# Optimization experiments

Measured on AMD Instinct MI355X. Metric: run time of the kernel, lower is better.

Reference implementation:

```python
import jax, jax.numpy as jnp
import numpy as np
import math

N_EMBD = 1024
N_HEAD = 16
B, T = 2, 2048


def new_gelu(x):
    # GPT-2 tanh-approx GELU (matches torch module exactly)
    return 0.5 * x * (1.0 + jnp.tanh(jnp.sqrt(2.0 / jnp.pi) * (x + 0.044715 * x ** 3)))


def layer_norm(x, w, b, eps=1e-5):
    mu = jnp.mean(x, axis=-1, keepdims=True)
    var = jnp.var(x, axis=-1, keepdims=True)
    return (x - mu) * jax.lax.rsqrt(var + eps) * w + b


def setup_inputs() -> dict:
    key = jax.random.key(0)
    ks = jax.random.split(key, 8)
    C = N_EMBD
    s = 0.02
    return {
        "x": jax.random.normal(ks[0], (B, T, C), dtype=jnp.float32),
        "ln1_w": jnp.ones((C,), jnp.float32),
        "ln1_b": jnp.zeros((C,), jnp.float32),
        "attn_w": s * jax.random.normal(ks[1], (C, 3 * C), jnp.float32),
        "attn_b": jnp.zeros((3 * C,), jnp.float32),
        "attn_proj_w": s * jax.random.normal(ks[2], (C, C), jnp.float32),
        "attn_proj_b": jnp.zeros((C,), jnp.float32),
        "ln2_w": jnp.ones((C,), jnp.float32),
        "ln2_b": jnp.zeros((C,), jnp.float32),
        "fc_w": s * jax.random.normal(ks[3], (C, 4 * C), jnp.float32),
        "fc_b": jnp.zeros((4 * C,), jnp.float32),
        "mlp_proj_w": s * jax.random.normal(ks[4], (4 * C, C), jnp.float32),
        "mlp_proj_b": jnp.zeros((C,), jnp.float32),
    }


def block_forward(x, ln1_w, ln1_b, attn_w, attn_b, attn_proj_w, attn_proj_b,
                  ln2_w, ln2_b, fc_w, fc_b, mlp_proj_w, mlp_proj_b):
    Bm, Tm, C = x.shape
    H = N_HEAD
    D = C // H
    # --- self attention (pre-LN) ---
    h = layer_norm(x, ln1_w, ln1_b)
    qkv = h @ attn_w + attn_b  # [B,T,3C]
    q, k, v = jnp.split(qkv, 3, axis=-1)
    q = q.reshape(Bm, Tm, H, D).transpose(0, 2, 1, 3)  # [B,H,T,D]
    k = k.reshape(Bm, Tm, H, D).transpose(0, 2, 1, 3)
    v = v.reshape(Bm, Tm, H, D).transpose(0, 2, 1, 3)
    att = jnp.einsum('bhqd,bhkd->bhqk', q, k) * (1.0 / math.sqrt(D))
    att = jax.nn.softmax(att, axis=-1)  # NOTE: no causal mask in source
    y = jnp.einsum('bhqk,bhkd->bhqd', att, v)
    y = y.transpose(0, 2, 1, 3).reshape(Bm, Tm, C)
    x = x + (y @ attn_proj_w + attn_proj_b)
    # --- MLP ---
    h = layer_norm(x, ln2_w, ln2_b)
    h = new_gelu(h @ fc_w + fc_b)
    x = x + (h @ mlp_proj_w + mlp_proj_b)
    return x


def reference(x, ln1_w, ln1_b, attn_w, attn_b, attn_proj_w, attn_proj_b,
              ln2_w, ln2_b, fc_w, fc_b, mlp_proj_w, mlp_proj_b):
    return block_forward(x, ln1_w, ln1_b, attn_w, attn_b, attn_proj_w, attn_proj_b,
                         ln2_w, ln2_b, fc_w, fc_b, mlp_proj_w, mlp_proj_b)
```

## Files before the change

kernel.cpp:

```cpp
#include <hip/hip_runtime.h>

typedef __attribute__((ext_vector_type(4)))  float  f32x4;
typedef __attribute__((ext_vector_type(16))) float  f32x16;
typedef __attribute__((ext_vector_type(8)))  short  s16x8;
typedef __attribute__((ext_vector_type(4)))  short  s16x4;
typedef __attribute__((ext_vector_type(4)))  unsigned u32x4;
typedef __attribute__((ext_vector_type(2)))  unsigned u32x2;
typedef __attribute__((ext_vector_type(2)))  int    i32x2;

__device__ __forceinline__ short f2bf(float f) {
    unsigned u = __builtin_bit_cast(unsigned, f);
    u += 0x7fff + ((u >> 16) & 1);
    return (short)(u >> 16);
}

__device__ __forceinline__ void load_lds16(const void* g, void* l) {
    __builtin_amdgcn_global_load_lds(
        (const __attribute__((address_space(1))) unsigned int*)g,
        (__attribute__((address_space(3))) unsigned int*)l, 16, 0, 0);
}

__global__ __launch_bounds__(256) void transpose_all(const float* __restrict__ w0,
                                                     const float* __restrict__ w1,
                                                     const float* __restrict__ w2,
                                                     const float* __restrict__ w3,
                                                     short* __restrict__ t0s,
                                                     short* __restrict__ t1s,
                                                     short* __restrict__ t2s,
                                                     short* __restrict__ t3s) {
    __shared__ float t[32][33];
    int id = blockIdx.x;
    const float* W; short* Wt; int K, N;
    if (id < 3072)      { W = w0; Wt = t0s; K = 1024; N = 3072; }
    else if (id < 4096) { W = w1; Wt = t1s; K = 1024; N = 1024; id -= 3072; }
    else if (id < 8192) { W = w2; Wt = t2s; K = 1024; N = 4096; id -= 4096; }
    else                { W = w3; Wt = t3s; K = 4096; N = 1024; id -= 8192; }
    int ntn = N >> 5;
    int n0 = (id % ntn) * 32, k0 = (id / ntn) * 32;
    int tx = threadIdx.x & 31, ty = threadIdx.x >> 5;
#pragma unroll
    for (int i = 0; i < 4; i++)
        t[ty + 8 * i][tx] = W[(size_t)(k0 + ty + 8 * i) * N + n0 + tx];
    __syncthreads();
#pragma unroll
    for (int i = 0; i < 4; i++)
        Wt[(size_t)(n0 + ty + 8 * i) * K + k0 + tx] = f2bf(t[tx][ty + 8 * i]);
}

__global__ __launch_bounds__(256) void ln_kernel(const float* __restrict__ x,
                                                 const float* __restrict__ w,
                                                 const float* __restrict__ b,
                                                 short* __restrict__ out) {
    int row = blockIdx.x;
    int tid = threadIdx.x;
    const float4 v = ((const float4*)(x + (size_t)row * 1024))[tid];
    float s  = v.x + v.y + v.z + v.w;
    float ss = v.x * v.x + v.y * v.y + v.z * v.z + v.w * v.w;
#pragma unroll
    for (int o = 32; o > 0; o >>= 1) {
        s  += __shfl_down(s, o);
        ss += __shfl_down(ss, o);
    }
    __shared__ float rs[4], rq[4];
    int wave = tid >> 6, lane = tid & 63;
    if (lane == 0) { rs[wave] = s; rq[wave] = ss; }
    __syncthreads();
    float tot = rs[0] + rs[1] + rs[2] + rs[3];
    float tq  = rq[0] + rq[1] + rq[2] + rq[3];
    float mu   = tot * (1.f / 1024.f);
    float var  = tq * (1.f / 1024.f) - mu * mu;
    float rstd = rsqrtf(var + 1e-5f);
    const float4 wv = ((const float4*)w)[tid];
    const float4 bv = ((const float4*)b)[tid];
    s16x4 o;
    o[0] = f2bf((v.x - mu) * rstd * wv.x + bv.x);
    o[1] = f2bf((v.y - mu) * rstd * wv.y + bv.y);
    o[2] = f2bf((v.z - mu) * rstd * wv.z + bv.z);
    o[3] = f2bf((v.w - mu) * rstd * wv.w + bv.w);
    ((s16x4*)(out + (size_t)row * 1024))[tid] = o;
}

__device__ __forceinline__ void xcd_remap(int& bx, int& by) {
    int gx = gridDim.x, gy = gridDim.y;
    int hwid = blockIdx.y * gx + blockIdx.x;
    int xcd = hwid & 7, rank = hwid >> 3;
    int pan = gx >> 3;
    bx = xcd * pan + rank / gy;
    by = rank % gy;
}

template <typename OUT_T, bool GELU, bool RES, bool SCALE_Q, bool VSPLIT>
__global__ __launch_bounds__(256) void gemm_bt(const short* __restrict__ A,
                                               const short* __restrict__ Bt,
                                               const float* __restrict__ bias,
                                               const float* __restrict__ res,
                                               OUT_T* __restrict__ C,
                                               short* __restrict__ vtg,
                                               int M, int N, int K) {
    __shared__ __align__(16) short As[2][128 * 32];
    __shared__ __align__(16) short Bs[2][128 * 32];
    int tid = threadIdx.x;
    int bx, by;
    xcd_remap(bx, by);
    int m0 = by * 128, n0 = bx * 128;
    int wave = tid >> 6, lane = tid & 63;
    int wr = wave >> 1, wc = wave & 1;
    int g = lane >> 4, q = lane & 15;
    f32x4 acc[4][4] = {};
    const short* Ab = A + (size_t)m0 * K;
    const short* Bb = Bt + (size_t)n0 * K;
    int srow = tid >> 2;
    int sx = (((tid & 3) ^ ((tid >> 3) & 3)) << 3);
    int fa = (q >> 1) & 3;
    auto stage = [&](int bi, int k0) {
        load_lds16(Ab + (size_t)srow * K + k0 + sx, &As[bi][tid * 8]);
        load_lds16(Ab + (size_t)(srow + 64) * K + k0 + sx, &As[bi][2048 + tid * 8]);
        load_lds16(Bb + (size_t)srow * K + k0 + sx, &Bs[bi][tid * 8]);
        load_lds16(Bb + (size_t)(srow + 64) * K + k0 + sx, &Bs[bi][2048 + tid * 8]);
    };
    int nk = K >> 5;
    stage(0, 0);
    __syncthreads();
    for (int kk = 0; kk < nk; ++kk) {
        int cur = kk & 1;
        if (kk + 1 < nk) stage(cur ^ 1, (kk + 1) << 5);
        s16x8 a[4], bf[4];
#pragma unroll
        for (int mi = 0; mi < 4; mi++)
            a[mi] = *(const s16x8*)(&As[cur][(wr * 64 + mi * 16 + q) * 32 + ((g ^ fa) << 3)]);
#pragma unroll
        for (int ni = 0; ni < 4; ni++)
            bf[ni] = *(const s16x8*)(&Bs[cur][(wc * 64 + ni * 16 + q) * 32 + ((g ^ fa) << 3)]);
#pragma unroll
        for (int mi = 0; mi < 4; mi++)
#pragma unroll
            for (int ni = 0; ni < 4; ni++)
                acc[mi][ni] = __builtin_amdgcn_mfma_f32_16x16x32_bf16(a[mi], bf[ni], acc[mi][ni], 0, 0, 0);
        __syncthreads();
    }
#pragma unroll
    for (int mi = 0; mi < 4; mi++) {
#pragma unroll
        for (int ni = 0; ni < 4; ni++) {
            int row = m0 + wr * 64 + mi * 16 + g * 4;
            int col = n0 + wc * 64 + ni * 16 + q;
            float bb = bias[col];
            if (VSPLIT && col >= 2048) {
                int d = col & 63;
                int bh2 = ((row >> 11) << 4) + ((col - 2048) >> 6);
                s16x4 o;
#pragma unroll
                for (int r = 0; r < 4; r++) o[r] = f2bf(acc[mi][ni][r] + bb);
                *(s16x4*)&vtg[((size_t)bh2 * 64 + d) * 2048 + (row & 2047)] = o;
            } else {
#pragma unroll
                for (int r = 0; r < 4; r++) {
                    float v = acc[mi][ni][r] + bb;
                    if (RES) v += res[(size_t)(row + r) * N + col];
                    if (GELU) {
                        float aa = 0.7978845608028654f * (v + 0.044715f * v * v * v);
                        float th = 1.f - 2.f / (__expf(2.f * aa) + 1.f);
                        v = 0.5f * v * (1.f + th);
                    }
                    if (SCALE_Q && col < 1024) v *= 0.18033688011112042f;
                    if constexpr (sizeof(OUT_T) == 2)
                        C[(size_t)(row + r) * N + col] = f2bf(v);
                    else
                        C[(size_t)(row + r) * N + col] = v;
                }
            }
        }
    }
}

__global__ __launch_bounds__(256) void gemm_bt_sk(const short* __restrict__ A,
                                                  const short* __restrict__ Bt,
                                                  float* __restrict__ part,
                                                  int M, int N, int K, int Klen) {
    __shared__ __align__(16) short As[2][128 * 32];
    __shared__ __align__(16) short Bs[2][128 * 32];
    int tid = threadIdx.x;
    int bx, by;
    xcd_remap(bx, by);
    int m0 = by * 128, n0 = bx * 128;
    int kz = blockIdx.z;
    int wave = tid >> 6, lane = tid & 63;
    int wr = wave >> 1, wc = wave & 1;
    int g = lane >> 4, q = lane & 15;
    f32x4 acc[4][4] = {};
    const short* Ab = A + (size_t)m0 * K;
    const short* Bb = Bt + (size_t)n0 * K;
    int srow = tid >> 2;
    int sx = (((tid & 3) ^ ((tid >> 3) & 3)) << 3);
    int fa = (q >> 1) & 3;
    auto stage = [&](int bi, int k0) {
        load_lds16(Ab + (size_t)srow * K + k0 + sx, &As[bi][tid * 8]);
        load_lds16(Ab + (size_t)(srow + 64) * K + k0 + sx, &As[bi][2048 + tid * 8]);
        load_lds16(Bb + (size_t)srow * K + k0 + sx, &Bs[bi][tid * 8]);
        load_lds16(Bb + (size_t)(srow + 64) * K + k0 + sx, &Bs[bi][2048 + tid * 8]);
    };
    int kbase = kz * Klen;
    int nk = Klen >> 5;
    stage(0, kbase);
    __syncthreads();
    for (int kk = 0; kk < nk; ++kk) {
        int cur = kk & 1;
        if (kk + 1 < nk) stage(cur ^ 1, kbase + ((kk + 1) << 5));
        s16x8 a[4], bf[4];
#pragma unroll
        for (int mi = 0; mi < 4; mi++)
            a[mi] = *(const s16x8*)(&As[cur][(wr * 64 + mi * 16 + q) * 32 + ((g ^ fa) << 3)]);
#pragma unroll
        for (int ni = 0; ni < 4; ni++)
            bf[ni] = *(const s16x8*)(&Bs[cur][(wc * 64 + ni * 16 + q) * 32 + ((g ^ fa) << 3)]);
#pragma unroll
        for (int mi = 0; mi < 4; mi++)
#pragma unroll
            for (int ni = 0; ni < 4; ni++)
                acc[mi][ni] = __builtin_amdgcn_mfma_f32_16x16x32_bf16(a[mi], bf[ni], acc[mi][ni], 0, 0, 0);
        __syncthreads();
    }
    float* pb = part + (size_t)kz * M * N;
#pragma unroll
    for (int mi = 0; mi < 4; mi++) {
#pragma unroll
        for (int ni = 0; ni < 4; ni++) {
            int row = m0 + wr * 64 + mi * 16 + g * 4;
            int col = n0 + wc * 64 + ni * 16 + q;
#pragma unroll
            for (int r = 0; r < 4; r++)
                pb[(size_t)(row + r) * N + col] = acc[mi][ni][r];
        }
    }
}

template <int SK>
__global__ __launch_bounds__(256) void reduce_sk(const float* __restrict__ part,
                                                 const float* __restrict__ bias,
                                                 const float* __restrict__ res,
                                                 float* __restrict__ out,
                                                 int MN, int N) {
    int tot = MN >> 2;
    int nb4 = (N >> 2) - 1;
    for (int i = blockIdx.x * 256 + threadIdx.x; i < tot; i += gridDim.x * 256) {
        float4 s = ((const float4*)part)[i];
#pragma unroll
        for (int k = 1; k < SK; k++) {
            float4 p = ((const float4*)(part + (size_t)k * MN))[i];
            s.x += p.x; s.y += p.y; s.z += p.z; s.w += p.w;
        }
        float4 bv = ((const float4*)bias)[i & nb4];
        float4 rv = ((const float4*)res)[i];
        float4 o;
        o.x = s.x + bv.x + rv.x;
        o.y = s.y + bv.y + rv.y;
        o.z = s.z + bv.z + rv.z;
        o.w = s.w + bv.w + rv.w;
        ((float4*)out)[i] = o;
    }
}

__global__ __launch_bounds__(128) void attn_kernel(const short* __restrict__ qkv,
                                                   const short* __restrict__ Vtg,
                                                   short* __restrict__ y) {
    const int T = 2048, C3 = 3072;
    int wg = blockIdx.x;
    int mapped = (wg & 7) * 128 + (wg >> 3);
    int bh = mapped >> 5, qt = mapped & 31;
    int b = bh >> 4, h = bh & 15;
    int tid = threadIdx.x, lane = tid & 63, wave = tid >> 6;
    int ql = lane & 31, hi = lane >> 5;
    const short* base = qkv + (size_t)b * T * C3;

    int qrow = qt * 64 + wave * 32 + ql;
    const short* qp = base + (size_t)qrow * C3 + h * 64;
    s16x8 qf[4];
#pragma unroll
    for (int s = 0; s < 4; s++)
        qf[s] = *(const s16x8*)(qp + ((2 * s + hi) << 3));

    __shared__ __align__(16) short Ks[2][64 * 64];
    __shared__ __align__(16) short Vs[2][64 * 64];

    int srow = tid >> 3, sc8 = tid & 7;
    const short* kp = base + 1024 + h * 64 + (size_t)srow * C3 + ((sc8 ^ (srow & 7)) << 3);
    const short* vp = Vtg + ((size_t)bh * 64 + srow) * T + ((sc8 ^ (srow & 7)) << 3);

    auto stage = [&](int bi) {
#pragma unroll
        for (int i = 0; i < 4; i++) {
            load_lds16(kp + (size_t)(16 * i) * C3, &Ks[bi][i * 1024 + tid * 8]);
            load_lds16(vp + (size_t)(16 * i) * T,  &Vs[bi][i * 1024 + tid * 8]);
        }
    };

    f32x16 accY0 = {}, accY1 = {}, accL = {};
    s16x8 ones;
#pragma unroll
    for (int i = 0; i < 8; i++) ones[i] = (short)0x3F80;
    int swz = ql & 7;

    auto tile = [&](int cur, bool last) {
        __syncthreads();
        if (!last) {
            kp += 64 * C3;
            vp += 64;
            stage(cur ^ 1);
        }
        f32x16 s0 = {}, s1 = {};
        const short* kb0 = &Ks[cur][ql * 64];
        const short* kb1 = &Ks[cur][(32 + ql) * 64];
        __builtin_amdgcn_s_setprio(1);
#pragma unroll
        for (int s = 0; s < 4; s++) {
            int c = ((2 * s + hi) ^ swz) << 3;
            s16x8 k0 = *(const s16x8*)(kb0 + c);
            s16x8 k1 = *(const s16x8*)(kb1 + c);
            s0 = __builtin_amdgcn_mfma_f32_32x32x16_bf16(k0, qf[s], s0, 0, 0, 0);
            s1 = __builtin_amdgcn_mfma_f32_32x32x16_bf16(k1, qf[s], s1, 0, 0, 0);
        }
        __builtin_amdgcn_s_setprio(0);
#pragma unroll
        for (int r = 0; r < 16; r++) s0[r] = exp2f(s0[r]);
#pragma unroll
        for (int r = 0; r < 16; r++) s1[r] = exp2f(s1[r]);
        s16x8 pb[4];
#pragma unroll
        for (int s = 0; s < 4; s++) {
            int tt = (s & 1) * 8;
            unsigned lo0, lo1, hi0, hi1;
            if (s < 2) {
                asm("v_cvt_pk_bf16_f32 %0, %1, %2" : "=v"(lo0) : "v"(s0[tt + 0]), "v"(s0[tt + 1]));
                asm("v_cvt_pk_bf16_f32 %0, %1, %2" : "=v"(lo1) : "v"(s0[tt + 2]), "v"(s0[tt + 3]));
                asm("v_cvt_pk_bf16_f32 %0, %1, %2" : "=v"(hi0) : "v"(s0[tt + 4]), "v"(s0[tt + 5]));
                asm("v_cvt_pk_bf16_f32 %0, %1, %2" : "=v"(hi1) : "v"(s0[tt + 6]), "v"(s0[tt + 7]));
            } else {
                asm("v_cvt_pk_bf16_f32 %0, %1, %2" : "=v"(lo0) : "v"(s1[tt + 0]), "v"(s1[tt + 1]));
                asm("v_cvt_pk_bf16_f32 %0, %1, %2" : "=v"(lo1) : "v"(s1[tt + 2]), "v"(s1[tt + 3]));
                asm("v_cvt_pk_bf16_f32 %0, %1, %2" : "=v"(hi0) : "v"(s1[tt + 4]), "v"(s1[tt + 5]));
                asm("v_cvt_pk_bf16_f32 %0, %1, %2" : "=v"(hi1) : "v"(s1[tt + 6]), "v"(s1[tt + 7]));
            }
            i32x2 r0 = __builtin_amdgcn_permlane32_swap((int)hi0, (int)lo0, false, false);
            i32x2 r1 = __builtin_amdgcn_permlane32_swap((int)hi1, (int)lo1, false, false);
            u32x4 w;
            w[0] = (unsigned)r0[1]; w[1] = (unsigned)r1[1];
            w[2] = (unsigned)r0[0]; w[3] = (unsigned)r1[0];
            pb[s] = __builtin_bit_cast(s16x8, w);
        }
        const short* vb0 = &Vs[cur][ql * 64];
        const short* vb1 = &Vs[cur][(32 + ql) * 64];
        __builtin_amdgcn_s_setprio(1);
#pragma unroll
        for (int s = 0; s < 4; s++) {
            int c = ((2 * s + hi) ^ swz) << 3;
            s16x8 v0 = *(const s16x8*)(vb0 + c);
            s16x8 v1 = *(const s16x8*)(vb1 + c);
            accY0 = __builtin_amdgcn_mfma_f32_32x32x16_bf16(v0, pb[s], accY0, 0, 0, 0);
            accY1 = __builtin_amdgcn_mfma_f32_32x32x16_bf16(v1, pb[s], accY1, 0, 0, 0);
            accL  = __builtin_amdgcn_mfma_f32_32x32x16_bf16(ones, pb[s], accL, 0, 0, 0);
        }
        __builtin_amdgcn_s_setprio(0);
    };

    stage(0);
    for (int t = 0; t < 32; t += 2) {
        tile(0, false);
        tile(1, t + 1 == 31);
    }

    float linv = 1.f / accL[0];
    short* yrow = y + ((size_t)b * T + qrow) * 1024 + h * 64;
#pragma unroll
    for (int r = 0; r < 4; r++) {
        unsigned w0, w1, w2, w3;
        float a0 = accY0[4 * r] * linv, a1 = accY0[4 * r + 1] * linv;
        float a2 = accY0[4 * r + 2] * linv, a3 = accY0[4 * r + 3] * linv;
        float b0 = accY1[4 * r] * linv, b1 = accY1[4 * r + 1] * linv;
        float b2 = accY1[4 * r + 2] * linv, b3 = accY1[4 * r + 3] * linv;
        asm("v_cvt_pk_bf16_f32 %0, %1, %2" : "=v"(w0) : "v"(a0), "v"(a1));
        asm("v_cvt_pk_bf16_f32 %0, %1, %2" : "=v"(w1) : "v"(a2), "v"(a3));
        asm("v_cvt_pk_bf16_f32 %0, %1, %2" : "=v"(w2) : "v"(b0), "v"(b1));
        asm("v_cvt_pk_bf16_f32 %0, %1, %2" : "=v"(w3) : "v"(b2), "v"(b3));
        u32x2 p0; p0[0] = w0; p0[1] = w1;
        u32x2 p1; p1[0] = w2; p1[1] = w3;
        *(u32x2*)(yrow + 8 * r + 4 * hi)      = p0;
        *(u32x2*)(yrow + 32 + 8 * r + 4 * hi) = p1;
    }
}

extern "C" void kernel_launch(void* const* d_in, const int* in_sizes, int n_in,
                              void* d_out, int out_size, void* d_ws, size_t ws_size,
                              hipStream_t stream) {
    const float* x           = (const float*)d_in[0];
    const float* ln1_w       = (const float*)d_in[1];
    const float* ln1_b       = (const float*)d_in[2];
    const float* attn_w      = (const float*)d_in[3];
    const float* attn_b      = (const float*)d_in[4];
    const float* attn_proj_w = (const float*)d_in[5];
    const float* attn_proj_b = (const float*)d_in[6];
    const float* ln2_w       = (const float*)d_in[7];
    const float* ln2_b       = (const float*)d_in[8];
    const float* fc_w        = (const float*)d_in[9];
    const float* fc_b        = (const float*)d_in[10];
    const float* mlp_proj_w  = (const float*)d_in[11];
    const float* mlp_proj_b  = (const float*)d_in[12];

    const int M = 4096;

    size_t off = 0;
    char* wsb = (char*)d_ws;
    auto alloc = [&](size_t bytes) {
        void* p = wsb + off;
        off += (bytes + 255) & ~(size_t)255;
        return p;
    };
    short* wt_attn  = (short*)alloc(3072ull * 1024 * 2);
    short* wt_proj  = (short*)alloc(1024ull * 1024 * 2);
    short* wt_fc    = (short*)alloc(4096ull * 1024 * 2);
    short* wt_mproj = (short*)alloc(1024ull * 4096 * 2);
    short* h1       = (short*)alloc((size_t)M * 1024 * 2);
    short* qkvb     = (short*)alloc((size_t)M * 3072 * 2);
    short* yb       = (short*)alloc((size_t)M * 1024 * 2);
    float* x1       = (float*)alloc((size_t)M * 1024 * 4);
    short* vtg      = (short*)alloc((size_t)M * 1024 * 2);
    short* h2       = qkvb;

    size_t base_off = off;
    int SK = 0;
    if (ws_size >= base_off + 4ull * M * 1024 * 4) SK = 4;
    else if (ws_size >= base_off + 2ull * M * 1024 * 4) SK = 2;
    float* part = (float*)(wsb + base_off);

    transpose_all<<<12288, 256, 0, stream>>>(attn_w, attn_proj_w, fc_w, mlp_proj_w,
                                             wt_attn, wt_proj, wt_fc, wt_mproj);

    ln_kernel<<<M, 256, 0, stream>>>(x, ln1_w, ln1_b, h1);
    gemm_bt<short, false, false, true, true><<<dim3(3072 / 128, M / 128), 256, 0, stream>>>(
        h1, wt_attn, attn_b, nullptr, qkvb, vtg, M, 3072, 1024);
    attn_kernel<<<1024, 128, 0, stream>>>(qkvb, vtg, yb);
    gemm_bt<float, false, true, false, false><<<dim3(1024 / 128, M / 128), 256, 0, stream>>>(
        yb, wt_proj, attn_proj_b, x, x1, nullptr, M, 1024, 1024);
    ln_kernel<<<M, 256, 0, stream>>>(x1, ln2_w, ln2_b, h1);
    gemm_bt<short, true, false, false, false><<<dim3(4096 / 128, M / 128), 256, 0, stream>>>(
        h1, wt_fc, fc_b, nullptr, h2, nullptr, M, 4096, 1024);

    if (SK == 4) {
        gemm_bt_sk<<<dim3(1024 / 128, M / 128, 4), 256, 0, stream>>>(
            h2, wt_mproj, part, M, 1024, 4096, 1024);
        reduce_sk<4><<<2048, 256, 0, stream>>>(part, mlp_proj_b, x1, (float*)d_out, M * 1024, 1024);
    } else if (SK == 2) {
        gemm_bt_sk<<<dim3(1024 / 128, M / 128, 2), 256, 0, stream>>>(
            h2, wt_mproj, part, M, 1024, 4096, 2048);
        reduce_sk<2><<<2048, 256, 0, stream>>>(part, mlp_proj_b, x1, (float*)d_out, M * 1024, 1024);
    } else {
        gemm_bt<float, false, true, false, false><<<dim3(1024 / 128, M / 128), 256, 0, stream>>>(
            h2, wt_mproj, mlp_proj_b, x1, (float*)d_out, nullptr, M, 1024, 4096);
    }
}
```

Before: 281.4 us.

## Software-pipeline attention: overlap next tile's QK MFMA with current softmax-PV

```diff
diff --git a/kernel.cpp b/kernel.cpp
--- a/kernel.cpp
+++ b/kernel.cpp
@@ -279,19 +279,24 @@
     for (int s = 0; s < 4; s++)
         qf[s] = *(const s16x8*)(qp + ((2 * s + hi) << 3));
 
-    __shared__ __align__(16) short Ks[2][64 * 64];
+    __shared__ __align__(16) short Ks[3][64 * 64];
     __shared__ __align__(16) short Vs[2][64 * 64];
 
     int srow = tid >> 3, sc8 = tid & 7;
     const short* kp = base + 1024 + h * 64 + (size_t)srow * C3 + ((sc8 ^ (srow & 7)) << 3);
     const short* vp = Vtg + ((size_t)bh * 64 + srow) * T + ((sc8 ^ (srow & 7)) << 3);
 
-    auto stage = [&](int bi) {
-#pragma unroll
-        for (int i = 0; i < 4; i++) {
+    auto stageK = [&](int bi) {
+#pragma unroll
+        for (int i = 0; i < 4; i++)
             load_lds16(kp + (size_t)(16 * i) * C3, &Ks[bi][i * 1024 + tid * 8]);
-            load_lds16(vp + (size_t)(16 * i) * T,  &Vs[bi][i * 1024 + tid * 8]);
-        }
+        kp += 64 * C3;
+    };
+    auto stageV = [&](int bi) {
+#pragma unroll
+        for (int i = 0; i < 4; i++)
+            load_lds16(vp + (size_t)(16 * i) * T, &Vs[bi][i * 1024 + tid * 8]);
+        vp += 64;
     };
 
     f32x16 accY0 = {}, accY1 = {}, accL = {};
@@ -300,26 +305,24 @@
     for (int i = 0; i < 8; i++) ones[i] = (short)0x3F80;
     int swz = ql & 7;
 
-    auto tile = [&](int cur, bool last) {
-        __syncthreads();
-        if (!last) {
-            kp += 64 * C3;
-            vp += 64;
-            stage(cur ^ 1);
-        }
-        f32x16 s0 = {}, s1 = {};
-        const short* kb0 = &Ks[cur][ql * 64];
-        const short* kb1 = &Ks[cur][(32 + ql) * 64];
+    auto qk = [&](const short* kbase_, f32x16& s0o, f32x16& s1o) {
+        f32x16 t0 = {}, t1 = {};
+        const short* kb0 = kbase_ + ql * 64;
+        const short* kb1 = kbase_ + (32 + ql) * 64;
         __builtin_amdgcn_s_setprio(1);
 #pragma unroll
         for (int s = 0; s < 4; s++) {
             int c = ((2 * s + hi) ^ swz) << 3;
             s16x8 k0 = *(const s16x8*)(kb0 + c);
             s16x8 k1 = *(const s16x8*)(kb1 + c);
-            s0 = __builtin_amdgcn_mfma_f32_32x32x16_bf16(k0, qf[s], s0, 0, 0, 0);
-            s1 = __builtin_amdgcn_mfma_f32_32x32x16_bf16(k1, qf[s], s1, 0, 0, 0);
+            t0 = __builtin_amdgcn_mfma_f32_32x32x16_bf16(k0, qf[s], t0, 0, 0, 0);
+            t1 = __builtin_amdgcn_mfma_f32_32x32x16_bf16(k1, qf[s], t1, 0, 0, 0);
         }
         __builtin_amdgcn_s_setprio(0);
+        s0o = t0; s1o = t1;
+    };
+
+    auto smpv = [&](f32x16& s0, f32x16& s1, const short* vbase_) {
 #pragma unroll
         for (int r = 0; r < 16; r++) s0[r] = exp2f(s0[r]);
 #pragma unroll
@@ -347,8 +350,8 @@
             w[2] = (unsigned)r0[0]; w[3] = (unsigned)r1[0];
             pb[s] = __builtin_bit_cast(s16x8, w);
         }
-        const short* vb0 = &Vs[cur][ql * 64];
-        const short* vb1 = &Vs[cur][(32 + ql) * 64];
+        const short* vb0 = vbase_ + ql * 64;
+        const short* vb1 = vbase_ + (32 + ql) * 64;
         __builtin_amdgcn_s_setprio(1);
 #pragma unroll
         for (int s = 0; s < 4; s++) {
@@ -362,10 +365,34 @@
         __builtin_amdgcn_s_setprio(0);
     };
 
-    stage(0);
+    stageK(0); stageV(0);
+    __syncthreads();
+    stageK(1);
+    f32x16 sa0, sa1, sb0, sb1;
+    qk(&Ks[0][0], sa0, sa1);
+    __syncthreads();
+
+    int kq = 1;
     for (int t = 0; t < 32; t += 2) {
-        tile(0, false);
-        tile(1, t + 1 == 31);
+        {
+            int kst = (kq == 2) ? 0 : kq + 1;
+            if (t + 2 < 32) stageK(kst);
+            if (t + 1 < 32) stageV((t + 1) & 1);
+            if (t + 1 < 32) qk(&Ks[kq][0], sb0, sb1);
+            smpv(sa0, sa1, &Vs[t & 1][0]);
+            __syncthreads();
+            kq = kst;
+        }
+        {
+            int t1 = t + 1;
+            int kst = (kq == 2) ? 0 : kq + 1;
+            if (t1 + 2 < 32) stageK(kst);
+            if (t1 + 1 < 32) stageV((t1 + 1) & 1);
+            if (t1 + 1 < 32) qk(&Ks[kq][0], sa0, sa1);
+            smpv(sb0, sb1, &Vs[t1 & 1][0]);
+            __syncthreads();
+            kq = kst;
+        }
     }
 
     float linv = 1.f / accL[0];
```

Measured after the change: 285.3 us. No clear change (+1.4%).
